# Kernel tuning notes

Hardware: AMD Instinct MI355X
Metric: run time of the kernel (lower is better)

Reference implementation:

```python
import jax, jax.numpy as jnp
import numpy as np

B = 256          # batch size
N_PIXELS = 784   # 28*28, fixed in source
N_TIME = 200     # fixed in source
N_CHUNKS = 10
EPS = 1e-20
INPUT_FREQ = 5.0


def setup_inputs() -> dict:
    key = jax.random.key(0)
    ks = jax.random.split(key, 8)
    x_batch = jax.random.normal(ks[0], (B, N_PIXELS), dtype=jnp.float32)
    v = jax.random.normal(ks[1], (N_PIXELS,), dtype=jnp.float32)
    # complex scatter matrix (learned-ish random complex weights)
    scatter_real = jax.random.normal(ks[2], (N_PIXELS, N_TIME), dtype=jnp.float32)
    scatter_imag = jax.random.normal(ks[3], (N_PIXELS, N_TIME), dtype=jnp.float32)
    # time-domain input waveform: exp(i*f*t) * exp(-500*f^2*t^2)
    t = np.linspace(-3.0, 3.0, N_TIME)
    wf = np.exp(1j * INPUT_FREQ * t) * np.exp(-500.0 * INPUT_FREQ**2 * t**2)
    waveform_real = jnp.asarray(wf.real, dtype=jnp.float32)
    waveform_imag = jnp.asarray(wf.imag, dtype=jnp.float32)
    # noisy gaussian envelope in frequency domain (complex)
    f = np.arange(N_TIME)
    g = np.exp(-0.5 * ((f - N_TIME / 2.0) / 20.0) ** 2).astype(np.float32)
    env_real = jnp.asarray(g) + 0.05 * jax.random.normal(ks[4], (N_TIME,), dtype=jnp.float32)
    env_imag = 0.05 * jax.random.normal(ks[5], (N_TIME,), dtype=jnp.float32)
    # nn.Linear(10, 10)
    lin_w = jax.random.uniform(ks[6], (10, 10), dtype=jnp.float32,
                               minval=-1.0, maxval=1.0) / jnp.sqrt(10.0)
    lin_b = jax.random.uniform(ks[7], (10,), dtype=jnp.float32,
                               minval=-1.0, maxval=1.0) / jnp.sqrt(10.0)
    return {
        "x_batch": x_batch, "v": v,
        "scatter_real": scatter_real, "scatter_imag": scatter_imag,
        "env_real": env_real, "env_imag": env_imag,
        "waveform_real": waveform_real, "waveform_imag": waveform_imag,
        "lin_w": lin_w, "lin_b": lin_b,
    }


def reference(x_batch, v, scatter_real, scatter_imag, env_real, env_imag,
              waveform_real, waveform_imag, lin_w, lin_b):
    waveform = (waveform_real + 1j * waveform_imag).astype(jnp.complex64)   # [T]
    envelope = (env_real + 1j * env_imag).astype(jnp.complex64)             # [T]
    weights = (scatter_real + 1j * scatter_imag).astype(jnp.complex64)      # [P,T]
    # modulated_input = outer(x, waveform); E_scaled = E_in * v[:,None]
    xv = (x_batch * v).astype(jnp.complex64)                                # [B,P]
    E_scaled = xv[:, :, None] * waveform[None, None, :]                     # [B,P,T]
    # FFT over time, multiply by noisy gaussian envelope
    E_fft = jnp.fft.fft(E_scaled, axis=-1) * envelope                       # [B,P,T]
    # einsum('ij,ij->j') per sample -> batched 'bpt,pt->bt'
    s = jnp.einsum('bpt,pt->bt', E_fft, weights)                            # [B,T]
    r = jnp.fft.ifft(s, axis=-1).real                                       # [B,T]
    # 10 chunks of 20, max |.| per chunk via sqrt(x^2 + eps)
    chunks = r.reshape(x_batch.shape[0], N_CHUNKS, N_TIME // N_CHUNKS)
    chunk_max = jnp.max(jnp.sqrt(chunks * chunks + EPS), axis=-1)           # [B,10]
    return chunk_max @ lin_w.T + lin_b
```

## Files before the change

kernel.cpp:

```cpp
#include <hip/hip_runtime.h>
#include <math.h>

#define NB 256
#define NP 784
#define NT 200

static constexpr float TWO_PI = 6.28318530717958647692f;

template <int R, int PC>
__global__ __launch_bounds__(256) void gemm_kernel(
        const float* __restrict__ x,  const float* __restrict__ v,
        const float* __restrict__ sr, const float* __restrict__ si,
        const float* __restrict__ wr, const float* __restrict__ wi,
        const float* __restrict__ er, const float* __restrict__ ei,
        float2* __restrict__ wenv, float2* __restrict__ up)
{
    constexpr int CH = NP / PC;
    constexpr int GB = (NB / R) * PC;
    __shared__ __align__(16) float xvT[CH][R];
    __shared__ float2 ctbl[NT];

    const int tid = threadIdx.x;
    const int g   = blockIdx.x;

    if (g == GB) {
        if (tid < NT) {
            float s, c;
            sincosf(TWO_PI * (float)tid / (float)NT, &s, &c);
            ctbl[tid] = make_float2(c, s);
        }
        __syncthreads();
        if (tid < NT) {
            const int k = tid;
            float Ar = 0.f, Ai = 0.f;
            int m = 0;
            for (int n = 0; n < NT; ++n) {
                float2 cs = ctbl[m];
                float wrv = wr[n], wiv = wi[n];
                Ar += wrv * cs.x + wiv * cs.y;
                Ai += wiv * cs.x - wrv * cs.y;
                m += k; if (m >= NT) m -= NT;
            }
            float erv = er[k], eiv = ei[k];
            wenv[k] = make_float2(Ar * erv - Ai * eiv, Ar * eiv + Ai * erv);
        }
        return;
    }

    const int rg = g / PC, c = g % PC;
    const int r0 = rg * R;
    const int p0 = c * CH;

    for (int p = tid; p < CH; p += 256) {
        float vv = v[p0 + p];
        #pragma unroll
        for (int r = 0; r < R; ++r)
            xvT[p][r] = x[(size_t)(r0 + r) * NP + p0 + p] * vv;
    }
    __syncthreads();

    const int t = tid;
    if (t < NT) {
        float ar[R], ai[R];
        #pragma unroll
        for (int r = 0; r < R; ++r) { ar[r] = 0.f; ai[r] = 0.f; }
        const float* srp = sr + (size_t)p0 * NT + t;
        const float* sip = si + (size_t)p0 * NT + t;
        for (int j = 0; j < CH; ++j) {
            float srv = srp[(size_t)j * NT];
            float siv = sip[(size_t)j * NT];
            #pragma unroll
            for (int rr = 0; rr < R; rr += 4) {
                float4 xv = *(const float4*)&xvT[j][rr];
                ar[rr+0] += xv.x * srv;  ai[rr+0] += xv.x * siv;
                ar[rr+1] += xv.y * srv;  ai[rr+1] += xv.y * siv;
                ar[rr+2] += xv.z * srv;  ai[rr+2] += xv.z * siv;
                ar[rr+3] += xv.w * srv;  ai[rr+3] += xv.w * siv;
            }
        }
        #pragma unroll
        for (int r = 0; r < R; ++r)
            up[((size_t)c * NB + r0 + r) * NT + t] = make_float2(ar[r], ai[r]);
    }
}

__global__ __launch_bounds__(256) void epilogue_kernel(
        const float2* __restrict__ up, int pc,
        const float2* __restrict__ wenv,
        const float* __restrict__ lw, const float* __restrict__ lb,
        float* __restrict__ out)
{
    __shared__ float2 ctbl[NT];
    __shared__ float2 s2[NT];
    __shared__ float  rbuf[NT];
    __shared__ float  cm[10];

    const int b   = blockIdx.x;
    const int tid = threadIdx.x;

    if (tid < NT) {
        float s, c;
        sincosf(TWO_PI * (float)tid / (float)NT, &s, &c);
        ctbl[tid] = make_float2(c, s);
        float ur = 0.f, ui = 0.f;
        for (int cc = 0; cc < pc; ++cc) {
            float2 pv = up[((size_t)cc * NB + b) * NT + tid];
            ur += pv.x; ui += pv.y;
        }
        float2 W = wenv[tid];
        s2[tid] = make_float2(ur * W.x - ui * W.y, ur * W.y + ui * W.x);
    }
    __syncthreads();

    if (tid < NT) {
        const int n = tid;
        float acc = 0.f;
        int m = 0;
        for (int t2 = 0; t2 < NT; ++t2) {
            float2 cs = ctbl[m];
            float2 sv = s2[t2];
            acc += sv.x * cs.x - sv.y * cs.y;
            m += n; if (m >= NT) m -= NT;
        }
        rbuf[tid] = acc * (1.0f / (float)NT);
    }
    __syncthreads();

    if (tid < 10) {
        float mx = 0.f;
        #pragma unroll
        for (int q = 0; q < 20; ++q) {
            float xv = rbuf[tid * 20 + q];
            mx = fmaxf(mx, sqrtf(xv * xv + 1e-20f));
        }
        cm[tid] = mx;
    }
    __syncthreads();

    if (tid < 10) {
        float o = lb[tid];
        #pragma unroll
        for (int k = 0; k < 10; ++k)
            o += cm[k] * lw[tid * 10 + k];
        out[b * 10 + tid] = o;
    }
}

extern "C" void kernel_launch(void* const* d_in, const int* in_sizes, int n_in,
                              void* d_out, int out_size, void* d_ws, size_t ws_size,
                              hipStream_t stream)
{
    const float* x  = (const float*)d_in[0];
    const float* v  = (const float*)d_in[1];
    const float* sr = (const float*)d_in[2];
    const float* si = (const float*)d_in[3];
    const float* er = (const float*)d_in[4];
    const float* ei = (const float*)d_in[5];
    const float* wr = (const float*)d_in[6];
    const float* wi = (const float*)d_in[7];
    const float* lw = (const float*)d_in[8];
    const float* lb = (const float*)d_in[9];
    float* out = (float*)d_out;

    float2* wenv = (float2*)d_ws;
    float2* up   = (float2*)((char*)d_ws + 4096);
    const size_t base     = 4096;
    const size_t per_copy = (size_t)NB * NT * sizeof(float2);

    int pc;
    if (ws_size >= base + 8 * per_copy) {
        pc = 8;
        gemm_kernel<8, 8><<<dim3((NB/8)*8 + 1), dim3(256), 0, stream>>>(
            x, v, sr, si, wr, wi, er, ei, wenv, up);
    } else if (ws_size >= base + 4 * per_copy) {
        pc = 4;
        gemm_kernel<4, 4><<<dim3((NB/4)*4 + 1), dim3(256), 0, stream>>>(
            x, v, sr, si, wr, wi, er, ei, wenv, up);
    } else {
        pc = 1;
        gemm_kernel<4, 1><<<dim3((NB/4) + 1), dim3(256), 0, stream>>>(
            x, v, sr, si, wr, wi, er, ei, wenv, up);
    }
    epilogue_kernel<<<dim3(NB), dim3(256), 0, stream>>>(up, pc, wenv, lw, lb, out);
}
```

Measured before the change: 97.36 us.

## Split GEMM over 16 pixel chunks and use twiddle recurrence in inverse DFT

Adds a PC=16 configuration that splits the pixel reduction into 16 chunks, launching more blocks to fill the GPU. The partial-sum count becomes a template parameter in the epilogue so its reduction loop unrolls. The epilogue's inverse DFT drops the shared cosine table and generates twiddles with a complex-rotation recurrence, reading two spectrum values per float4. It also unrolls the GEMM pixel loop by 4. The trade-offs are more partial-sum traffic to reduce and some accumulated float error from the twiddle recurrence.

```diff
diff --git a/kernel.cpp b/kernel.cpp
--- a/kernel.cpp
+++ b/kernel.cpp
@@ -66,6 +66,7 @@
         for (int r = 0; r < R; ++r) { ar[r] = 0.f; ai[r] = 0.f; }
         const float* srp = sr + (size_t)p0 * NT + t;
         const float* sip = si + (size_t)p0 * NT + t;
+        #pragma unroll 4
         for (int j = 0; j < CH; ++j) {
             float srv = srp[(size_t)j * NT];
             float siv = sip[(size_t)j * NT];
@@ -84,14 +85,14 @@
     }
 }
 
+template <int PC>
 __global__ __launch_bounds__(256) void epilogue_kernel(
-        const float2* __restrict__ up, int pc,
+        const float2* __restrict__ up,
         const float2* __restrict__ wenv,
         const float* __restrict__ lw, const float* __restrict__ lb,
         float* __restrict__ out)
 {
-    __shared__ float2 ctbl[NT];
-    __shared__ float2 s2[NT];
+    __shared__ __align__(16) float2 s2[NT];
     __shared__ float  rbuf[NT];
     __shared__ float  cm[10];
 
@@ -99,11 +100,9 @@
     const int tid = threadIdx.x;
 
     if (tid < NT) {
-        float s, c;
-        sincosf(TWO_PI * (float)tid / (float)NT, &s, &c);
-        ctbl[tid] = make_float2(c, s);
         float ur = 0.f, ui = 0.f;
-        for (int cc = 0; cc < pc; ++cc) {
+        #pragma unroll
+        for (int cc = 0; cc < PC; ++cc) {
             float2 pv = up[((size_t)cc * NB + b) * NT + tid];
             ur += pv.x; ui += pv.y;
         }
@@ -113,14 +112,19 @@
     __syncthreads();
 
     if (tid < NT) {
-        const int n = tid;
-        float acc = 0.f;
-        int m = 0;
-        for (int t2 = 0; t2 < NT; ++t2) {
-            float2 cs = ctbl[m];
-            float2 sv = s2[t2];
-            acc += sv.x * cs.x - sv.y * cs.y;
-            m += n; if (m >= NT) m -= NT;
+        float rs, rc;
+        sincosf(TWO_PI * (float)tid / (float)NT, &rs, &rc);
+        float cr = 1.f, ci = 0.f, acc = 0.f;
+        const float4* sv4 = (const float4*)s2;
+        #pragma unroll 5
+        for (int h = 0; h < NT / 2; ++h) {
+            float4 two = sv4[h];
+            acc += two.x * cr - two.y * ci;
+            float nr = cr * rc - ci * rs;
+            float ni = cr * rs + ci * rc;
+            acc += two.z * nr - two.w * ni;
+            cr = nr * rc - ni * rs;
+            ci = nr * rs + ni * rc;
         }
         rbuf[tid] = acc * (1.0f / (float)NT);
     }
@@ -167,19 +171,21 @@
     const size_t base     = 4096;
     const size_t per_copy = (size_t)NB * NT * sizeof(float2);
 
-    int pc;
-    if (ws_size >= base + 8 * per_copy) {
-        pc = 8;
+    if (ws_size >= base + 16 * per_copy) {
+        gemm_kernel<8, 16><<<dim3((NB/8)*16 + 1), dim3(256), 0, stream>>>(
+            x, v, sr, si, wr, wi, er, ei, wenv, up);
+        epilogue_kernel<16><<<dim3(NB), dim3(256), 0, stream>>>(up, wenv, lw, lb, out);
+    } else if (ws_size >= base + 8 * per_copy) {
         gemm_kernel<8, 8><<<dim3((NB/8)*8 + 1), dim3(256), 0, stream>>>(
             x, v, sr, si, wr, wi, er, ei, wenv, up);
+        epilogue_kernel<8><<<dim3(NB), dim3(256), 0, stream>>>(up, wenv, lw, lb, out);
     } else if (ws_size >= base + 4 * per_copy) {
-        pc = 4;
         gemm_kernel<4, 4><<<dim3((NB/4)*4 + 1), dim3(256), 0, stream>>>(
             x, v, sr, si, wr, wi, er, ei, wenv, up);
+        epilogue_kernel<4><<<dim3(NB), dim3(256), 0, stream>>>(up, wenv, lw, lb, out);
     } else {
-        pc = 1;
         gemm_kernel<4, 1><<<dim3((NB/4) + 1), dim3(256), 0, stream>>>(
             x, v, sr, si, wr, wi, er, ei, wenv, up);
+        epilogue_kernel<1><<<dim3(NB), dim3(256), 0, stream>>>(up, wenv, lw, lb, out);
     }
-    epilogue_kernel<<<dim3(NB), dim3(256), 0, stream>>>(up, pc, wenv, lw, lb, out);
 }
```

Measured after the change: 91.52 us. 1.06x faster.
